# Optimization experiments

Measured on AMD Instinct MI355X. Metric: run time of the kernel, lower is better.

Reference implementation:

```python
import jax, jax.numpy as jnp
import numpy as np

B, L, D, H, F, NL = 112, 128, 768, 12, 3072, 3
E = D // H  # head dim = 64
BN_EPS = 1e-5


def _bn(x, gamma, beta):
    # torch BatchNorm1d applied on x.permute(0,2,1): per-channel (d_model) stats over batch+seq
    mean = jnp.mean(x, axis=(0, 1), keepdims=True)
    var = jnp.var(x, axis=(0, 1), keepdims=True)
    return (x - mean) * jax.lax.rsqrt(var + BN_EPS) * gamma + beta


def setup_inputs() -> dict:
    key = jax.random.key(0)
    ks = jax.random.split(key, 10)
    s = 0.02
    inp = {
        "x": jax.random.normal(ks[0], (B, L, D), jnp.float32),
        "attn_bias": jax.random.normal(ks[1], (B, L, L, H), jnp.float32) * 0.1,
        "Wq": jax.random.normal(ks[2], (NL, D, D), jnp.float32) * s,
        "bq": jnp.zeros((NL, D), jnp.float32),
        "Wk": jax.random.normal(ks[3], (NL, D, D), jnp.float32) * s,
        "bk": jnp.zeros((NL, D), jnp.float32),
        "Wv": jax.random.normal(ks[4], (NL, D, D), jnp.float32) * s,
        "bv": jnp.zeros((NL, D), jnp.float32),
        "Wo": jax.random.normal(ks[5], (NL, D, D), jnp.float32) * s,
        "bo": jnp.zeros((NL, D), jnp.float32),
        "W1": jax.random.normal(ks[6], (NL, F, D), jnp.float32) * s,  # conv1 k=1 == Linear
        "b1": jnp.zeros((NL, F), jnp.float32),
        "W2": jax.random.normal(ks[7], (NL, D, F), jnp.float32) * s,  # conv2 k=1 == Linear
        "b2": jnp.zeros((NL, D), jnp.float32),
        "g1": jnp.ones((NL, D), jnp.float32),
        "be1": jnp.zeros((NL, D), jnp.float32),
        "g2": jnp.ones((NL, D), jnp.float32),
        "be2": jnp.zeros((NL, D), jnp.float32),
        "gf": jnp.ones((D,), jnp.float32),
        "bef": jnp.zeros((D,), jnp.float32),
    }
    return inp


def reference(x, attn_bias, Wq, bq, Wk, bk, Wv, bv, Wo, bo,
              W1, b1, W2, b2, g1, be1, g2, be2, gf, bef):
    scale = 1.0 / float(np.sqrt(E))
    bias_bhls = jnp.transpose(attn_bias, (0, 3, 1, 2))  # [B,H,L,S]
    for l in range(NL):
        q = (x @ Wq[l].T + bq[l]).reshape(B, L, H, E)
        k = (x @ Wk[l].T + bk[l]).reshape(B, L, H, E)
        v = (x @ Wv[l].T + bv[l]).reshape(B, L, H, E)
        scores = jnp.einsum('blhe,bshe->bhls', q, k)  # O(L^2) score tensor
        A = jax.nn.softmax(scores * scale + bias_bhls, axis=-1)
        V = jnp.einsum('bhls,bshd->blhd', A, v).reshape(B, L, D)
        new_x = V @ Wo[l].T + bo[l]
        x = _bn(x + new_x, g1[l], be1[l])
        y = jax.nn.gelu(x @ W1[l].T + b1[l], approximate=False)
        y = y @ W2[l].T + b2[l]
        x = _bn(x + y, g2[l], be2[l])
    return _bn(x, gf, bef)  # Encoder final BatchNorm1d(d_model)
```

## Files before the change

### kernel.cpp

```cpp
#include <hip/hip_runtime.h>

#define NB 112
#define SEQ 128
#define DM 768
#define NH 12
#define HD 64
#define FF 3072
#define NLAYER 3
#define MTOK (NB*SEQ)
#define QKVN (3*DM)
#define HEADTOT (NB*NH)
#define QSZ ((size_t)HEADTOT*SEQ*HD)

typedef unsigned short u16;
typedef __attribute__((ext_vector_type(8))) short short8;
typedef __attribute__((ext_vector_type(4))) float f32x4;
typedef __attribute__((ext_vector_type(4))) unsigned short us4;

__device__ __forceinline__ u16 f2bf(float f){
  unsigned u = __builtin_bit_cast(unsigned, f);
  u += 0x7FFFu + ((u >> 16) & 1u);
  return (u16)(u >> 16);
}
__device__ __forceinline__ float bf2f(u16 b){
  unsigned u = ((unsigned)b) << 16;
  return __builtin_bit_cast(float, u);
}
__device__ __forceinline__ unsigned cvt_pk_bf16(float lo, float hi){
  unsigned r;
  asm("v_cvt_pk_bf16_f32 %0, %1, %2" : "=v"(r) : "v"(lo), "v"(hi));
  return r;
}
__device__ __forceinline__ float gelu_t(float x){
  const float t = -1.5957691216057308f * x * __builtin_fmaf(0.044715f, x*x, 1.0f);
  return __fdividef(x, 1.0f + __expf(t));
}

__device__ __forceinline__ void gl_lds16(const void* g, void* l){
  __builtin_amdgcn_global_load_lds((const __attribute__((address_space(1))) unsigned*)g,
                                   (__attribute__((address_space(3))) unsigned*)l, 16, 0, 0);
}

template<int EPI>
__global__ __launch_bounds__(512, 2)
void gemm_bt(const u16* __restrict__ A, const u16* __restrict__ W,
             const float* __restrict__ bias, u16* __restrict__ obf,
             float* __restrict__ of32, const u16* __restrict__ res,
             float* __restrict__ p1, float* __restrict__ p2,
             int M, int N, int K, int Nt, int TPB)
{
  __shared__ __align__(16) char smem[131072];
  const int tid = threadIdx.x;
  const int w = tid >> 6, lane = tid & 63;
  const int wm = w >> 2, wn = w & 3;
  const int fr = lane & 15, fg = lane >> 4;
  const int fko = fg * 8;
  const int grid = gridDim.x;
  const int q8 = grid >> 3, r8 = grid & 7;
  const int xcd = blockIdx.x & 7, pos = blockIdx.x >> 3;
  const int start = xcd < r8 ? xcd * (q8 + 1) : r8 * (q8 + 1) + (xcd - r8) * q8;
  const int swz = start + pos;
  const int nt = K >> 6;
  const int tot = TPB * nt;
  const int l3 = lane >> 3;
  const int k16s = ((lane & 7) ^ l3) * 8;
  int rowAK[2][2], rowBK[2][2];
  #pragma unroll
  for (int mh = 0; mh < 2; mh++)
    #pragma unroll
    for (int j = 0; j < 2; j++)
      rowAK[mh][j] = (mh*64 + j*128 + w*8 + l3) * K;
  #pragma unroll
  for (int h = 0; h < 2; h++)
    #pragma unroll
    for (int j = 0; j < 2; j++)
      rowBK[h][j] = (h*128 + (w + j*8)*8 + l3) * K;

  auto stA2 = [&](int bb, int mh, int soff) {
    const u16* g0 = A + (size_t)soff + rowAK[mh][0] + k16s;
    const u16* g1 = A + (size_t)soff + rowAK[mh][1] + k16s;
    char* d = smem + bb*65536 + (mh*64 + w*8)*128;
    gl_lds16(g0, d);
    gl_lds16(g1, d + 16384);
  };
  auto stB2 = [&](int bb, int h, int soff) {
    const u16* g0 = W + (size_t)soff + rowBK[h][0] + k16s;
    const u16* g1 = W + (size_t)soff + rowBK[h][1] + k16s;
    char* d = smem + bb*65536 + 32768 + (h*128 + w*8)*128;
    gl_lds16(g0, d);
    gl_lds16(g1, d + 8192);
  };
  const int axor = (fr & 7) << 4;
  auto rdA2 = [&](int bb, int mh, int kh, int mf) -> short8 {
    const int row = wm*128 + mh*64 + mf*16 + fr;
    return *(const short8*)(smem + bb*65536 + row*128 + (((kh*32 + fko)*2) ^ axor));
  };
  auto rdB2 = [&](int bb, int kh, int nf) -> short8 {
    const int row = wn*64 + nf*16 + fr;
    return *(const short8*)(smem + bb*65536 + 32768 + row*128 + (((kh*32 + fko)*2) ^ axor));
  };
  auto coord = [&](int r, int& bm, int& bn) {
    const int lin = swz * TPB + r;
    const int mI = lin / Nt;
    bm = mI * 256; bn = (lin - mI * Nt) * 256;
  };

  f32x4 acc[8][4] = {};

  auto epi = [&](int bm, int bn) {
    float bs[4] = {0,0,0,0}, bq[4] = {0,0,0,0};
    #pragma unroll
    for (int mi = 0; mi < 8; mi++) {
      #pragma unroll
      for (int ni = 0; ni < 4; ni++) {
        const int c = bn + wn*64 + ni*16 + fr;
        const int r0 = bm + wm*128 + (mi>>2)*64 + (mi&3)*16 + fg*4;
        const float bc = bias[c];
        float v[4];
        #pragma unroll
        for (int j = 0; j < 4; j++) v[j] = acc[mi][ni][j] + bc;
        if constexpr (EPI == 1) {
          #pragma unroll
          for (int j = 0; j < 4; j++) v[j] = gelu_t(v[j]);
          const unsigned p01 = cvt_pk_bf16(v[0], v[1]);
          const unsigned p23 = cvt_pk_bf16(v[2], v[3]);
          u16* d = obf + (size_t)r0 * N + c;
          d[0] = (u16)p01; d[N] = (u16)(p01 >> 16);
          d[2*N] = (u16)p23; d[3*N] = (u16)(p23 >> 16);
        } else if constexpr (EPI == 2) {
          #pragma unroll
          for (int j = 0; j < 4; j++) {
            const float y = v[j] + bf2f(res[(size_t)(r0+j) * N + c]);
            of32[(size_t)(r0+j) * N + c] = y;
            bs[ni] += y; bq[ni] += y * y;
          }
        } else {
          const int which = c / DM;
          const int cc = c - which * DM;
          const int hh = cc >> 6, e = cc & 63;
          const int bb = r0 >> 7, l = r0 & 127;
          const unsigned p01 = cvt_pk_bf16(v[0], v[1]);
          const unsigned p23 = cvt_pk_bf16(v[2], v[3]);
          u16* d = obf + (size_t)which * QSZ + ((size_t)(bb*NH + hh) * SEQ + l) * HD + e;
          d[0] = (u16)p01; d[HD] = (u16)(p01 >> 16);
          d[2*HD] = (u16)p23; d[3*HD] = (u16)(p23 >> 16);
        }
        acc[mi][ni] = (f32x4){0.f, 0.f, 0.f, 0.f};
      }
    }
    if constexpr (EPI == 2) {
      const int mIdx = bm >> 8;
      #pragma unroll
      for (int ni = 0; ni < 4; ni++) {
        float s = bs[ni], qq = bq[ni];
        s  += __shfl_xor(s, 16);  s  += __shfl_xor(s, 32);
        qq += __shfl_xor(qq, 16); qq += __shfl_xor(qq, 32);
        if (fg == 0) {
          const int c = bn + wn*64 + ni*16 + fr;
          p1[(mIdx*2 + wm) * N + c] = s;
          p2[(mIdx*2 + wm) * N + c] = qq;
        }
      }
    }
  };

  int r0t = 0, kt0 = 0, bm0, bn0; coord(0, bm0, bn0);
  int r1 = 0, kt1 = 1, bm1 = bm0, bn1 = bn0;
  int r2 = 0, kt2 = 2, bm2 = bm0;
  if (kt2 >= nt) { kt2 -= nt; r2 = 1; int d; if (r2 < TPB) coord(r2, bm2, d); }

  stA2(0, 0, bm0*K); stA2(0, 1, bm0*K);
  stB2(0, 0, bn0*K); stB2(0, 1, bn0*K);
  if (tot > 1) stA2(1, 0, bm1*K + kt1*64);
  asm volatile("s_waitcnt vmcnt(2)" ::: "memory");
  __builtin_amdgcn_s_barrier();

  short8 a0[4], a1[4], bk0[4], bk1[4];
  for (int it = 0; it < tot; ++it) {
    const int bufc = it & 1, nb = bufc ^ 1;
    const bool st1 = (it + 1 < tot), st2 = (it + 2 < tot);
    const int sB1 = bn1*K + kt1*64;
    const int sA1 = bm1*K + kt1*64;
    const int sA2 = bm2*K + kt2*64;
    #pragma unroll
    for (int i = 0; i < 4; i++) a0[i] = rdA2(bufc, 0, 0, i);
    #pragma unroll
    for (int i = 0; i < 4; i++) a1[i] = rdA2(bufc, 0, 1, i);
    #pragma unroll
    for (int i = 0; i < 4; i++) bk0[i] = rdB2(bufc, 0, i);
    #pragma unroll
    for (int i = 0; i < 4; i++) bk1[i] = rdB2(bufc, 1, i);
    if (st1) { stB2(nb, 0, sB1); stB2(nb, 1, sB1); }
    __builtin_amdgcn_s_barrier();
    asm volatile("s_waitcnt lgkmcnt(0)" ::: "memory");
    __builtin_amdgcn_sched_barrier(0);
    __builtin_amdgcn_s_setprio(1);
    #pragma unroll
    for (int mi = 0; mi < 4; mi++)
      #pragma unroll
      for (int ni = 0; ni < 4; ni++)
        acc[mi][ni] = __builtin_amdgcn_mfma_f32_16x16x32_bf16(a0[mi], bk0[ni], acc[mi][ni], 0, 0, 0);
    #pragma unroll
    for (int mi = 0; mi < 4; mi++)
      #pragma unroll
      for (int ni = 0; ni < 4; ni++)
        acc[mi][ni] = __builtin_amdgcn_mfma_f32_16x16x32_bf16(a1[mi], bk1[ni], acc[mi][ni], 0, 0, 0);
    __builtin_amdgcn_s_setprio(0);
    if (st1) { asm volatile("s_waitcnt vmcnt(4)" ::: "memory"); }
    else     { asm volatile("s_waitcnt vmcnt(0)" ::: "memory"); }
    __builtin_amdgcn_s_barrier();
    #pragma unroll
    for (int i = 0; i < 4; i++) a0[i] = rdA2(bufc, 1, 0, i);
    #pragma unroll
    for (int i = 0; i < 4; i++) a1[i] = rdA2(bufc, 1, 1, i);
    if (st2) stA2(bufc, 0, sA2);
    if (st1) stA2(nb, 1, sA1);
    __builtin_amdgcn_s_barrier();
    asm volatile("s_waitcnt lgkmcnt(0)" ::: "memory");
    __builtin_amdgcn_sched_barrier(0);
    __builtin_amdgcn_s_setprio(1);
    #pragma unroll
    for (int mi = 0; mi < 4; mi++)
      #pragma unroll
      for (int ni = 0; ni < 4; ni++)
        acc[4+mi][ni] = __builtin_amdgcn_mfma_f32_16x16x32_bf16(a0[mi], bk0[ni], acc[4+mi][ni], 0, 0, 0);
    #pragma unroll
    for (int mi = 0; mi < 4; mi++)
      #pragma unroll
      for (int ni = 0; ni < 4; ni++)
        acc[4+mi][ni] = __builtin_amdgcn_mfma_f32_16x16x32_bf16(a1[mi], bk1[ni], acc[4+mi][ni], 0, 0, 0);
    __builtin_amdgcn_s_setprio(0);
    if (st2)      { asm volatile("s_waitcnt vmcnt(4)" ::: "memory"); }
    else if (st1) { asm volatile("s_waitcnt vmcnt(2)" ::: "memory"); }
    __builtin_amdgcn_s_barrier();
    if (kt0 == nt - 1) {
      epi(bm0, bn0);
      kt0 = 0; r0t++;
      if (r0t < TPB) coord(r0t, bm0, bn0);
    } else kt0++;
    kt1++; if (kt1 == nt) { kt1 = 0; r1++; if (r1 < TPB) coord(r1, bm1, bn1); }
    kt2++; if (kt2 == nt) { kt2 = 0; r2++; if (r2 < TPB) { int d; coord(r2, bm2, d); } }
  }
}

__global__ __launch_bounds__(256)
void attn_kernel(const u16* __restrict__ qkvb, const u16* __restrict__ biasT,
                 u16* __restrict__ ab)
{
  const int h = blockIdx.x, b = blockIdx.y;
  const int tid = threadIdx.x, w = tid >> 6, lane = tid & 63;
  const int bh = b * NH + h;
  const u16* qp = qkvb + (size_t)bh * SEQ * HD;
  const u16* kp = qkvb + QSZ + (size_t)bh * SEQ * HD;
  const u16* vp = qkvb + 2 * QSZ + (size_t)bh * SEQ * HD;
  __shared__ __align__(16) u16 vT[HD * 136];
  __shared__ __align__(16) u16 P[SEQ * 136];
  {
    const int s = tid & 127, half = tid >> 7;
    #pragma unroll
    for (int rr = 0; rr < 4; rr++) {
      const int e0 = half * 32 + rr * 8;
      short8 v8 = *(const short8*)&vp[s * HD + e0];
      #pragma unroll
      for (int j = 0; j < 8; j++) vT[(e0 + j) * 136 + s] = (u16)v8[j];
    }
  }
  const int fr = lane & 15, fg = lane >> 4;
  f32x4 sacc[2][8] = {};
  #pragma unroll
  for (int ks = 0; ks < 2; ks++) {
    const int k0 = ks * 32 + fg * 8;
    short8 qf[2], kf[8];
    #pragma unroll
    for (int mi = 0; mi < 2; mi++) qf[mi] = *(const short8*)&qp[(w*32 + mi*16 + fr) * HD + k0];
    #pragma unroll
    for (int ni = 0; ni < 8; ni++) kf[ni] = *(const short8*)&kp[(ni*16 + fr) * HD + k0];
    #pragma unroll
    for (int mi = 0; mi < 2; mi++)
      #pragma unroll
      for (int ni = 0; ni < 8; ni++)
        sacc[mi][ni] = __builtin_amdgcn_mfma_f32_16x16x32_bf16(qf[mi], kf[ni], sacc[mi][ni], 0, 0, 0);
  }
  const u16* bt = biasT + (size_t)bh * SEQ * SEQ;
  #pragma unroll
  for (int mi = 0; mi < 2; mi++) {
    #pragma unroll
    for (int j = 0; j < 4; j++) {
      const int l = w*32 + mi*16 + fg*4 + j;
      float vals[8];
      float mx = -1e30f;
      #pragma unroll
      for (int ni = 0; ni < 8; ni++) {
        vals[ni] = sacc[mi][ni][j] * 0.125f + bf2f(bt[l * SEQ + ni*16 + fr]);
        mx = fmaxf(mx, vals[ni]);
      }
      #pragma unroll
      for (int d = 1; d < 16; d <<= 1) mx = fmaxf(mx, __shfl_xor(mx, d));
      float sum = 0.f;
      #pragma unroll
      for (int ni = 0; ni < 8; ni++) { vals[ni] = __expf(vals[ni] - mx); sum += vals[ni]; }
      #pragma unroll
      for (int d = 1; d < 16; d <<= 1) sum += __shfl_xor(sum, d);
      const float inv = 1.0f / sum;
      #pragma unroll
      for (int ni = 0; ni < 8; ni++) P[l * 136 + ni*16 + fr] = f2bf(vals[ni] * inv);
    }
  }
  __syncthreads();
  f32x4 oacc[2][4] = {};
  #pragma unroll
  for (int ss = 0; ss < 4; ss++) {
    const int s0 = ss * 32 + fg * 8;
    short8 pf[2], vf[4];
    #pragma unroll
    for (int mi = 0; mi < 2; mi++) pf[mi] = *(const short8*)&P[(w*32 + mi*16 + fr) * 136 + s0];
    #pragma unroll
    for (int ei = 0; ei < 4; ei++) vf[ei] = *(const short8*)&vT[(ei*16 + fr) * 136 + s0];
    #pragma unroll
    for (int mi = 0; mi < 2; mi++)
      #pragma unroll
      for (int ei = 0; ei < 4; ei++)
        oacc[mi][ei] = __builtin_amdgcn_mfma_f32_16x16x32_bf16(pf[mi], vf[ei], oacc[mi][ei], 0, 0, 0);
  }
  #pragma unroll
  for (int mi = 0; mi < 2; mi++)
    #pragma unroll
    for (int ei = 0; ei < 4; ei++)
      #pragma unroll
      for (int j = 0; j < 4; j++) {
        const int r = b * SEQ + w*32 + mi*16 + fg*4 + j;
        const int c = h * HD + ei*16 + fr;
        ab[(size_t)r * DM + c] = f2bf(oacc[mi][ei][j]);
      }
}

template<bool FINAL>
__global__ __launch_bounds__(256)
void bn_final(const float* __restrict__ p1, const float* __restrict__ p2,
              const float* __restrict__ ga, const float* __restrict__ be,
              const float* __restrict__ gb, const float* __restrict__ beb,
              float* __restrict__ sc, float* __restrict__ sh)
{
  const int c = blockIdx.x * 256 + threadIdx.x;
  float s = 0, q = 0;
  for (int i = 0; i < 112; i++) { s += p1[i * DM + c]; q += p2[i * DM + c]; }
  const float mean = s * (1.0f / MTOK);
  const float var = q * (1.0f / MTOK) - mean * mean;
  const float rstd = rsqrtf(var + 1e-5f);
  if constexpr (!FINAL) {
    const float g = ga[c] * rstd;
    sc[c] = g;
    sh[c] = be[c] - mean * g;
  } else {
    const float sc2 = ga[c] * rstd;
    const float sh2 = be[c] - mean * sc2;
    const float varf = sc2 * sc2 * var;
    const float meanf = sc2 * mean + sh2;
    const float scf = gb[c] * rsqrtf(varf + 1e-5f);
    const float shf = beb[c] - meanf * scf;
    sc[c] = scf * sc2;
    sh[c] = scf * sh2 + shf;
  }
}

template<int MODE>
__global__ __launch_bounds__(256)
void bn_apply(const float* __restrict__ xi, const float* __restrict__ sc,
              const float* __restrict__ sh, float* __restrict__ xo, u16* __restrict__ xb)
{
  const int i = blockIdx.x * 256 + threadIdx.x;
  const int cv = i % (DM / 4);
  float4 v = ((const float4*)xi)[i];
  const float4 s = ((const float4*)sc)[cv];
  const float4 h = ((const float4*)sh)[cv];
  float4 y;
  y.x = v.x * s.x + h.x; y.y = v.y * s.y + h.y;
  y.z = v.z * s.z + h.z; y.w = v.w * s.w + h.w;
  if constexpr (MODE == 1) {
    ((float4*)xo)[i] = y;
  } else {
    us4 pk; pk[0] = f2bf(y.x); pk[1] = f2bf(y.y); pk[2] = f2bf(y.z); pk[3] = f2bf(y.w);
    *(us4*)(xb + (size_t)i * 4) = pk;
  }
}

__global__ __launch_bounds__(256)
void conv_bf16(const float* __restrict__ s, u16* __restrict__ d, int n4)
{
  const int i = blockIdx.x * 256 + threadIdx.x;
  if (i >= n4) return;
  float4 v = ((const float4*)s)[i];
  us4 pk; pk[0] = f2bf(v.x); pk[1] = f2bf(v.y); pk[2] = f2bf(v.z); pk[3] = f2bf(v.w);
  *(us4*)(d + (size_t)i * 4) = pk;
}

__global__ __launch_bounds__(256)
void conv_qkvw(const float* __restrict__ wq, const float* __restrict__ wk,
               const float* __restrict__ wv, u16* __restrict__ d)
{
  const int i = blockIdx.x * 256 + threadIdx.x;
  const int per = QKVN * DM / 4;
  const int l = i / per;
  const int rem = i - l * per;
  const int r = rem / (DM / 4);
  const int cv = rem - r * (DM / 4);
  const float* srcrow;
  if (r < DM)          srcrow = wq + ((size_t)l * DM + r) * DM;
  else if (r < 2 * DM) srcrow = wk + ((size_t)l * DM + (r - DM)) * DM;
  else                 srcrow = wv + ((size_t)l * DM + (r - 2 * DM)) * DM;
  float4 v = ((const float4*)srcrow)[cv];
  us4 pk; pk[0] = f2bf(v.x); pk[1] = f2bf(v.y); pk[2] = f2bf(v.z); pk[3] = f2bf(v.w);
  *(us4*)(d + (size_t)i * 4) = pk;
}

__global__ __launch_bounds__(256)
void conv_bias_qkv(const float* __restrict__ bq, const float* __restrict__ bk,
                   const float* __restrict__ bv, float* __restrict__ d)
{
  const int i = blockIdx.x * 256 + threadIdx.x;
  const int l = i / QKVN;
  const int r = i - l * QKVN;
  float v;
  if (r < DM)          v = bq[l * DM + r];
  else if (r < 2 * DM) v = bk[l * DM + r - DM];
  else                 v = bv[l * DM + r - 2 * DM];
  d[i] = v;
}

__global__ __launch_bounds__(256)
void bias_tr(const float* __restrict__ src, u16* __restrict__ dst)
{
  const int l = blockIdx.x, b = blockIdx.y;
  __shared__ float row[SEQ * NH];
  const float* s = src + ((size_t)b * SEQ + l) * SEQ * NH;
  for (int i = threadIdx.x; i < SEQ * NH; i += 256) row[i] = s[i];
  __syncthreads();
  for (int i = threadIdx.x; i < SEQ * NH; i += 256) {
    const int h = i >> 7, ss = i & 127;
    dst[((size_t)(b * NH + h) * SEQ + l) * SEQ + ss] = f2bf(row[ss * NH + h]);
  }
}

extern "C" void kernel_launch(void* const* d_in, const int* in_sizes, int n_in,
                              void* d_out, int out_size, void* d_ws, size_t ws_size,
                              hipStream_t stream)
{
  const float* x    = (const float*)d_in[0];
  const float* abia = (const float*)d_in[1];
  const float* Wq   = (const float*)d_in[2];
  const float* bq   = (const float*)d_in[3];
  const float* Wk   = (const float*)d_in[4];
  const float* bk   = (const float*)d_in[5];
  const float* Wv   = (const float*)d_in[6];
  const float* bv   = (const float*)d_in[7];
  const float* Wo   = (const float*)d_in[8];
  const float* bo   = (const float*)d_in[9];
  const float* W1   = (const float*)d_in[10];
  const float* b1   = (const float*)d_in[11];
  const float* W2   = (const float*)d_in[12];
  const float* b2   = (const float*)d_in[13];
  const float* g1   = (const float*)d_in[14];
  const float* be1  = (const float*)d_in[15];
  const float* g2   = (const float*)d_in[16];
  const float* be2  = (const float*)d_in[17];
  const float* gf   = (const float*)d_in[18];
  const float* bef  = (const float*)d_in[19];
  float* out = (float*)d_out;

  char* ws = (char*)d_ws;
  size_t off = 0;
  auto alloc = [&](size_t n) -> char* {
    char* p = ws + off;
    off = (off + n + 255) & ~(size_t)255;
    return p;
  };
  u16*  wqkv  = (u16*)alloc((size_t)3 * QKVN * DM * 2);
  u16*  wo    = (u16*)alloc((size_t)3 * DM * DM * 2);
  u16*  w1    = (u16*)alloc((size_t)3 * FF * DM * 2);
  u16*  w2    = (u16*)alloc((size_t)3 * DM * FF * 2);
  float* bqkv = (float*)alloc((size_t)3 * QKVN * 4);
  u16*  xb    = (u16*)alloc((size_t)MTOK * DM * 2);
  u16*  ab    = (u16*)alloc((size_t)MTOK * DM * 2);
  u16*  big   = (u16*)alloc((size_t)MTOK * FF * 2);
  u16*  biasT = (u16*)alloc((size_t)HEADTOT * SEQ * SEQ * 2);
  float* p1   = (float*)alloc((size_t)112 * DM * 4);
  float* p2   = (float*)alloc((size_t)112 * DM * 4);
  float* sc   = (float*)alloc(DM * 4);
  float* sh   = (float*)alloc(DM * 4);
  if (off > ws_size) return;

  conv_qkvw<<<5184, 256, 0, stream>>>(Wq, Wk, Wv, wqkv);
  conv_bf16<<<1728, 256, 0, stream>>>(Wo, wo, 3 * DM * DM / 4);
  conv_bf16<<<6912, 256, 0, stream>>>(W1, w1, 3 * FF * DM / 4);
  conv_bf16<<<6912, 256, 0, stream>>>(W2, w2, 3 * DM * FF / 4);
  conv_bias_qkv<<<27, 256, 0, stream>>>(bq, bk, bv, bqkv);
  bias_tr<<<dim3(SEQ, NB), 256, 0, stream>>>(abia, biasT);
  conv_bf16<<<MTOK * DM / 4 / 256, 256, 0, stream>>>(x, xb, MTOK * DM / 4);

  auto gemm = [&](int epi, const u16* Ap, const u16* Wp, const float* bp,
                  u16* ob, float* o32, const u16* rs, int M, int N, int K) {
    const int Nt = N / 256;
    const int tiles = (M / 256) * Nt;
    const int tpb = (tiles + 255) / 256;
    const int grid = tiles / tpb;
    if (epi == 1)
      gemm_bt<1><<<grid, 512, 0, stream>>>(Ap, Wp, bp, ob, o32, rs, p1, p2, M, N, K, Nt, tpb);
    else if (epi == 2)
      gemm_bt<2><<<grid, 512, 0, stream>>>(Ap, Wp, bp, ob, o32, rs, p1, p2, M, N, K, Nt, tpb);
    else
      gemm_bt<3><<<grid, 512, 0, stream>>>(Ap, Wp, bp, ob, o32, rs, p1, p2, M, N, K, Nt, tpb);
  };

  for (int l = 0; l < NLAYER; l++) {
    gemm(3, xb, wqkv + (size_t)l * QKVN * DM, bqkv + l * QKVN, big, nullptr, nullptr,
         MTOK, QKVN, DM);
    attn_kernel<<<dim3(NH, NB), 256, 0, stream>>>(big, biasT, ab);
    gemm(2, ab, wo + (size_t)l * DM * DM, bo + l * DM, nullptr, out, xb,
         MTOK, DM, DM);
    bn_final<false><<<3, 256, 0, stream>>>(p1, p2, g1 + l * DM, be1 + l * DM,
                                           nullptr, nullptr, sc, sh);
    bn_apply<0><<<MTOK * DM / 4 / 256, 256, 0, stream>>>(out, sc, sh, nullptr, xb);
    gemm(1, xb, w1 + (size_t)l * FF * DM, b1 + l * FF, big, nullptr, nullptr,
         MTOK, FF, DM);
    gemm(2, big, w2 + (size_t)l * DM * FF, b2 + l * DM, nullptr, out, xb,
         MTOK, DM, FF);
    if (l < NLAYER - 1) {
      bn_final<false><<<3, 256, 0, stream>>>(p1, p2, g2 + l * DM, be2 + l * DM,
                                             nullptr, nullptr, sc, sh);
      bn_apply<0><<<MTOK * DM / 4 / 256, 256, 0, stream>>>(out, sc, sh, nullptr, xb);
    } else {
      bn_final<true><<<3, 256, 0, stream>>>(p1, p2, g2 + l * DM, be2 + l * DM,
                                            gf, bef, sc, sh);
      bn_apply<1><<<MTOK * DM / 4 / 256, 256, 0, stream>>>(out, sc, sh, out, nullptr);
    }
  }
}
```

Measured before the change: 1.151 ms.

## Shrink GEMM tiles to 128x128 with 256-thread blocks and fixed grid

Replaces the 256x256 tile, 512-thread, 128KB-LDS GEMM with a 128x128 tile, 256-thread kernel that stages 32-wide K slices into a 32KB double buffer. The launch grid is fixed at 672 blocks, each doing an equal number of tiles. The BN partial-sum buffers double to 224 rows to match the smaller M tiles. The aim is higher occupancy (3 blocks per CU) and better load balance across CUs, at the cost of less data reuse per tile and more barriers per unit of K.

```diff
diff --git a/kernel.cpp b/kernel.cpp
--- a/kernel.cpp
+++ b/kernel.cpp
@@ -42,80 +42,64 @@
 }
 
 template<int EPI>
-__global__ __launch_bounds__(512, 2)
+__global__ __launch_bounds__(256, 3)
 void gemm_bt(const u16* __restrict__ A, const u16* __restrict__ W,
              const float* __restrict__ bias, u16* __restrict__ obf,
              float* __restrict__ of32, const u16* __restrict__ res,
              float* __restrict__ p1, float* __restrict__ p2,
              int M, int N, int K, int Nt, int TPB)
 {
-  __shared__ __align__(16) char smem[131072];
+  __shared__ __align__(16) char smem[32768];
   const int tid = threadIdx.x;
   const int w = tid >> 6, lane = tid & 63;
-  const int wm = w >> 2, wn = w & 3;
+  const int wm = w >> 1, wn = w & 1;
   const int fr = lane & 15, fg = lane >> 4;
-  const int fko = fg * 8;
   const int grid = gridDim.x;
-  const int q8 = grid >> 3, r8 = grid & 7;
+  const int q8 = grid >> 3;
   const int xcd = blockIdx.x & 7, pos = blockIdx.x >> 3;
-  const int start = xcd < r8 ? xcd * (q8 + 1) : r8 * (q8 + 1) + (xcd - r8) * q8;
-  const int swz = start + pos;
-  const int nt = K >> 6;
+  const int swz = xcd * q8 + pos;
+  const int nt = K >> 5;
   const int tot = TPB * nt;
-  const int l3 = lane >> 3;
-  const int k16s = ((lane & 7) ^ l3) * 8;
-  int rowAK[2][2], rowBK[2][2];
-  #pragma unroll
-  for (int mh = 0; mh < 2; mh++)
-    #pragma unroll
-    for (int j = 0; j < 2; j++)
-      rowAK[mh][j] = (mh*64 + j*128 + w*8 + l3) * K;
-  #pragma unroll
-  for (int h = 0; h < 2; h++)
-    #pragma unroll
-    for (int j = 0; j < 2; j++)
-      rowBK[h][j] = (h*128 + (w + j*8)*8 + l3) * K;
-
-  auto stA2 = [&](int bb, int mh, int soff) {
-    const u16* g0 = A + (size_t)soff + rowAK[mh][0] + k16s;
-    const u16* g1 = A + (size_t)soff + rowAK[mh][1] + k16s;
-    char* d = smem + bb*65536 + (mh*64 + w*8)*128;
-    gl_lds16(g0, d);
-    gl_lds16(g1, d + 16384);
-  };
-  auto stB2 = [&](int bb, int h, int soff) {
-    const u16* g0 = W + (size_t)soff + rowBK[h][0] + k16s;
-    const u16* g1 = W + (size_t)soff + rowBK[h][1] + k16s;
-    char* d = smem + bb*65536 + 32768 + (h*128 + w*8)*128;
-    gl_lds16(g0, d);
-    gl_lds16(g1, d + 8192);
-  };
-  const int axor = (fr & 7) << 4;
-  auto rdA2 = [&](int bb, int mh, int kh, int mf) -> short8 {
-    const int row = wm*128 + mh*64 + mf*16 + fr;
-    return *(const short8*)(smem + bb*65536 + row*128 + (((kh*32 + fko)*2) ^ axor));
-  };
-  auto rdB2 = [&](int bb, int kh, int nf) -> short8 {
+  const int rowt = tid >> 2;
+  const int kofs = ((tid & 3) ^ (rowt & 3)) * 8;
+  auto stage = [&](int bb, int bm_, int bn_, int kt_) {
+    const int kbase = kt_ * 32 + kofs;
+    #pragma unroll
+    for (int j = 0; j < 2; j++) {
+      const u16* ga = A + (size_t)(bm_ + j*64 + rowt) * K + kbase;
+      gl_lds16(ga, smem + bb*16384 + j*4096 + tid*16);
+    }
+    #pragma unroll
+    for (int j = 0; j < 2; j++) {
+      const u16* gb = W + (size_t)(bn_ + j*64 + rowt) * K + kbase;
+      gl_lds16(gb, smem + bb*16384 + 8192 + j*4096 + tid*16);
+    }
+  };
+  auto rdA = [&](int bb, int mf) -> short8 {
+    const int row = wm*64 + mf*16 + fr;
+    return *(const short8*)(smem + bb*16384 + row*64 + ((fg ^ (row & 3)) * 16));
+  };
+  auto rdB = [&](int bb, int nf) -> short8 {
     const int row = wn*64 + nf*16 + fr;
-    return *(const short8*)(smem + bb*65536 + 32768 + row*128 + (((kh*32 + fko)*2) ^ axor));
+    return *(const short8*)(smem + bb*16384 + 8192 + row*64 + ((fg ^ (row & 3)) * 16));
   };
   auto coord = [&](int r, int& bm, int& bn) {
     const int lin = swz * TPB + r;
     const int mI = lin / Nt;
-    bm = mI * 256; bn = (lin - mI * Nt) * 256;
-  };
-
-  f32x4 acc[8][4] = {};
+    bm = mI * 128; bn = (lin - mI * Nt) * 128;
+  };
+
+  f32x4 acc[4][4] = {};
 
   auto epi = [&](int bm, int bn) {
     float bs[4] = {0,0,0,0}, bq[4] = {0,0,0,0};
     #pragma unroll
-    for (int mi = 0; mi < 8; mi++) {
-      #pragma unroll
-      for (int ni = 0; ni < 4; ni++) {
-        const int c = bn + wn*64 + ni*16 + fr;
-        const int r0 = bm + wm*128 + (mi>>2)*64 + (mi&3)*16 + fg*4;
-        const float bc = bias[c];
+    for (int ni = 0; ni < 4; ni++) {
+      const int c = bn + wn*64 + ni*16 + fr;
+      const float bc = bias[c];
+      #pragma unroll
+      for (int mi = 0; mi < 4; mi++) {
+        const int r0 = bm + wm*64 + mi*16 + fg*4;
         float v[4];
         #pragma unroll
         for (int j = 0; j < 4; j++) v[j] = acc[mi][ni][j] + bc;
@@ -149,7 +133,7 @@
       }
     }
     if constexpr (EPI == 2) {
-      const int mIdx = bm >> 8;
+      const int mIdx = bm >> 7;
       #pragma unroll
       for (int ni = 0; ni < 4; ni++) {
         float s = bs[ni], qq = bq[ni];
@@ -165,81 +149,41 @@
   };
 
   int r0t = 0, kt0 = 0, bm0, bn0; coord(0, bm0, bn0);
-  int r1 = 0, kt1 = 1, bm1 = bm0, bn1 = bn0;
-  int r2 = 0, kt2 = 2, bm2 = bm0;
-  if (kt2 >= nt) { kt2 -= nt; r2 = 1; int d; if (r2 < TPB) coord(r2, bm2, d); }
-
-  stA2(0, 0, bm0*K); stA2(0, 1, bm0*K);
-  stB2(0, 0, bn0*K); stB2(0, 1, bn0*K);
-  if (tot > 1) stA2(1, 0, bm1*K + kt1*64);
-  asm volatile("s_waitcnt vmcnt(2)" ::: "memory");
+  int r2 = 0, kt2 = 2, bm2 = bm0, bn2 = bn0;
+
+  stage(0, bm0, bn0, 0);
+  stage(1, bm0, bn0, 1);
+  asm volatile("s_waitcnt vmcnt(4)" ::: "memory");
   __builtin_amdgcn_s_barrier();
 
-  short8 a0[4], a1[4], bk0[4], bk1[4];
-  for (int it = 0; it < tot; ++it) {
-    const int bufc = it & 1, nb = bufc ^ 1;
-    const bool st1 = (it + 1 < tot), st2 = (it + 2 < tot);
-    const int sB1 = bn1*K + kt1*64;
-    const int sA1 = bm1*K + kt1*64;
-    const int sA2 = bm2*K + kt2*64;
-    #pragma unroll
-    for (int i = 0; i < 4; i++) a0[i] = rdA2(bufc, 0, 0, i);
-    #pragma unroll
-    for (int i = 0; i < 4; i++) a1[i] = rdA2(bufc, 0, 1, i);
-    #pragma unroll
-    for (int i = 0; i < 4; i++) bk0[i] = rdB2(bufc, 0, i);
-    #pragma unroll
-    for (int i = 0; i < 4; i++) bk1[i] = rdB2(bufc, 1, i);
-    if (st1) { stB2(nb, 0, sB1); stB2(nb, 1, sB1); }
-    __builtin_amdgcn_s_barrier();
+  short8 a[4], b[4];
+  for (int t = 0; t < tot; ++t) {
+    const int buf = t & 1;
+    const bool st1 = (t + 1 < tot), st2 = (t + 2 < tot);
+    #pragma unroll
+    for (int i = 0; i < 4; i++) a[i] = rdA(buf, i);
+    #pragma unroll
+    for (int i = 0; i < 4; i++) b[i] = rdB(buf, i);
     asm volatile("s_waitcnt lgkmcnt(0)" ::: "memory");
     __builtin_amdgcn_sched_barrier(0);
+    __builtin_amdgcn_s_barrier();
+    if (st2) stage(buf, bm2, bn2, kt2);
     __builtin_amdgcn_s_setprio(1);
     #pragma unroll
     for (int mi = 0; mi < 4; mi++)
       #pragma unroll
       for (int ni = 0; ni < 4; ni++)
-        acc[mi][ni] = __builtin_amdgcn_mfma_f32_16x16x32_bf16(a0[mi], bk0[ni], acc[mi][ni], 0, 0, 0);
-    #pragma unroll
-    for (int mi = 0; mi < 4; mi++)
-      #pragma unroll
-      for (int ni = 0; ni < 4; ni++)
-        acc[mi][ni] = __builtin_amdgcn_mfma_f32_16x16x32_bf16(a1[mi], bk1[ni], acc[mi][ni], 0, 0, 0);
-    __builtin_amdgcn_s_setprio(0);
-    if (st1) { asm volatile("s_waitcnt vmcnt(4)" ::: "memory"); }
-    else     { asm volatile("s_waitcnt vmcnt(0)" ::: "memory"); }
-    __builtin_amdgcn_s_barrier();
-    #pragma unroll
-    for (int i = 0; i < 4; i++) a0[i] = rdA2(bufc, 1, 0, i);
-    #pragma unroll
-    for (int i = 0; i < 4; i++) a1[i] = rdA2(bufc, 1, 1, i);
-    if (st2) stA2(bufc, 0, sA2);
-    if (st1) stA2(nb, 1, sA1);
-    __builtin_amdgcn_s_barrier();
-    asm volatile("s_waitcnt lgkmcnt(0)" ::: "memory");
-    __builtin_amdgcn_sched_barrier(0);
-    __builtin_amdgcn_s_setprio(1);
-    #pragma unroll
-    for (int mi = 0; mi < 4; mi++)
-      #pragma unroll
-      for (int ni = 0; ni < 4; ni++)
-        acc[4+mi][ni] = __builtin_amdgcn_mfma_f32_16x16x32_bf16(a0[mi], bk0[ni], acc[4+mi][ni], 0, 0, 0);
-    #pragma unroll
-    for (int mi = 0; mi < 4; mi++)
-      #pragma unroll
-      for (int ni = 0; ni < 4; ni++)
-        acc[4+mi][ni] = __builtin_amdgcn_mfma_f32_16x16x32_bf16(a1[mi], bk1[ni], acc[4+mi][ni], 0, 0, 0);
+        acc[mi][ni] = __builtin_amdgcn_mfma_f32_16x16x32_bf16(a[mi], b[ni], acc[mi][ni], 0, 0, 0);
     __builtin_amdgcn_s_setprio(0);
     if (st2)      { asm volatile("s_waitcnt vmcnt(4)" ::: "memory"); }
-    else if (st1) { asm volatile("s_waitcnt vmcnt(2)" ::: "memory"); }
+    else if (st1) { asm volatile("s_waitcnt vmcnt(0)" ::: "memory"); }
     __builtin_amdgcn_s_barrier();
     if (kt0 == nt - 1) {
       epi(bm0, bn0);
       kt0 = 0; r0t++;
       if (r0t < TPB) coord(r0t, bm0, bn0);
     } else kt0++;
-    kt1++; if (kt1 == nt) { kt1 = 0; r1++; if (r1 < TPB) coord(r1, bm1, bn1); }
-    kt2++; if (kt2 == nt) { kt2 = 0; r2++; if (r2 < TPB) { int d; coord(r2, bm2, d); } }
+    kt2++; if (kt2 == nt) { kt2 = 0; r2++; if (r2 < TPB) coord(r2, bm2, bn2); }
   }
 }
 
@@ -343,7 +287,7 @@
 {
   const int c = blockIdx.x * 256 + threadIdx.x;
   float s = 0, q = 0;
-  for (int i = 0; i < 112; i++) { s += p1[i * DM + c]; q += p2[i * DM + c]; }
+  for (int i = 0; i < 224; i++) { s += p1[i * DM + c]; q += p2[i * DM + c]; }
   const float mean = s * (1.0f / MTOK);
   const float var = q * (1.0f / MTOK) - mean * mean;
   const float rstd = rsqrtf(var + 1e-5f);
@@ -483,8 +427,8 @@
   u16*  ab    = (u16*)alloc((size_t)MTOK * DM * 2);
   u16*  big   = (u16*)alloc((size_t)MTOK * FF * 2);
   u16*  biasT = (u16*)alloc((size_t)HEADTOT * SEQ * SEQ * 2);
-  float* p1   = (float*)alloc((size_t)112 * DM * 4);
-  float* p2   = (float*)alloc((size_t)112 * DM * 4);
+  float* p1   = (float*)alloc((size_t)224 * DM * 4);
+  float* p2   = (float*)alloc((size_t)224 * DM * 4);
   float* sc   = (float*)alloc(DM * 4);
   float* sh   = (float*)alloc(DM * 4);
   if (off > ws_size) return;
@@ -499,16 +443,16 @@
 
   auto gemm = [&](int epi, const u16* Ap, const u16* Wp, const float* bp,
                   u16* ob, float* o32, const u16* rs, int M, int N, int K) {
-    const int Nt = N / 256;
-    const int tiles = (M / 256) * Nt;
-    const int tpb = (tiles + 255) / 256;
-    const int grid = tiles / tpb;
+    const int Nt = N / 128;
+    const int tiles = (M / 128) * Nt;
+    const int grid = 672;
+    const int tpb = tiles / grid;
     if (epi == 1)
-      gemm_bt<1><<<grid, 512, 0, stream>>>(Ap, Wp, bp, ob, o32, rs, p1, p2, M, N, K, Nt, tpb);
+      gemm_bt<1><<<grid, 256, 0, stream>>>(Ap, Wp, bp, ob, o32, rs, p1, p2, M, N, K, Nt, tpb);
     else if (epi == 2)
-      gemm_bt<2><<<grid, 512, 0, stream>>>(Ap, Wp, bp, ob, o32, rs, p1, p2, M, N, K, Nt, tpb);
+      gemm_bt<2><<<grid, 256, 0, stream>>>(Ap, Wp, bp, ob, o32, rs, p1, p2, M, N, K, Nt, tpb);
     else
-      gemm_bt<3><<<grid, 512, 0, stream>>>(Ap, Wp, bp, ob, o32, rs, p1, p2, M, N, K, Nt, tpb);
+      gemm_bt<3><<<grid, 256, 0, stream>>>(Ap, Wp, bp, ob, o32, rs, p1, p2, M, N, K, Nt, tpb);
   };
 
   for (int l = 0; l < NLAYER; l++) {
```

After: 1.315 ms. 1.14x slower.
